# Kernel optimization log

Measured on AMD Instinct MI355X. Metric: run time of the kernel, lower is better.

Reference implementation:

```python
import jax, jax.numpy as jnp
import numpy as np

S, B, E, H = 2048, 2, 1024, 16
D = E // H  # head_dim = 64


def setup_inputs() -> dict:
    key = jax.random.key(0)
    ks = jax.random.split(key, 5)
    sp = (2.0 / (E + E)) ** 0.5  # xavier-ish scale
    return {
        "x": jax.random.normal(ks[0], (S, B, E), dtype=jnp.float32),
        "wq": jax.random.normal(ks[1], (E, E), dtype=jnp.float32) * sp,
        "bq": jnp.zeros((E,), jnp.float32),
        "wk": jax.random.normal(ks[2], (E, E), dtype=jnp.float32) * sp,
        "bk": jnp.zeros((E,), jnp.float32),
        "wv": jax.random.normal(ks[3], (E, E), dtype=jnp.float32) * sp,
        "bv": jnp.zeros((E,), jnp.float32),
        "wo": jax.random.normal(ks[4], (E, E), dtype=jnp.float32) * sp,
        "bo": jnp.zeros((E,), jnp.float32),
    }


def reference(x, wq, bq, wk, bk, wv, bv, wo, bo):
    # x: (S, B, E), weights in torch Linear convention (out, in)
    scaling = jnp.float32(D ** -0.5)
    q = (jnp.einsum('ibe,fe->ibf', x, wq) + bq) * scaling
    k = jnp.einsum('ibe,fe->ibf', x, wk) + bk
    v = jnp.einsum('ibe,fe->ibf', x, wv) + bv
    q = q.reshape(S, B, H, D)
    k = k.reshape(S, B, H, D)
    v = v.reshape(S, B, H, D)
    # energy: (B, H, S_q, S_k)
    energy = jnp.einsum('ibnf,jbnf->bnij', q, k)
    causal = jnp.triu(jnp.ones((S, S), dtype=bool), k=1)  # True above diagonal
    energy = jnp.where(causal[None, None], -jnp.inf, energy)
    weights = jax.nn.softmax(energy, axis=-1)
    head_ctx = jnp.einsum('bnij,jbnf->ibnf', weights, v)
    context = head_ctx.reshape(S, B, E)
    out = jnp.einsum('ibe,fe->ibf', context, wo) + bo
    return out
```

## Files before the change

kernel.cpp:

```cpp
#include <hip/hip_runtime.h>
#include <hip/hip_bf16.h>
#include <stdint.h>

#define S_LEN 2048
#define BATCH 2
#define EMB   1024
#define NH    16
#define HD    64
#define LOG2E 1.4426950408889634f

typedef __bf16 bf16x8 __attribute__((ext_vector_type(8)));
typedef float  f32x4  __attribute__((ext_vector_type(4)));
typedef unsigned short ushort8 __attribute__((ext_vector_type(8)));

__device__ __forceinline__ unsigned short f2bf(float f) {
  __bf16 h = (__bf16)f;
  return __builtin_bit_cast(unsigned short, h);
}

__device__ __forceinline__ ushort8 cvt8(const float4 a, const float4 b) {
  ushort8 o;
  o[0]=f2bf(a.x); o[1]=f2bf(a.y); o[2]=f2bf(a.z); o[3]=f2bf(a.w);
  o[4]=f2bf(b.x); o[5]=f2bf(b.y); o[6]=f2bf(b.z); o[7]=f2bf(b.w);
  return o;
}

__device__ __forceinline__ unsigned long long pack4(const f32x4 v) {
  return  (unsigned long long)f2bf(v[0])
       | ((unsigned long long)f2bf(v[1]) << 16)
       | ((unsigned long long)f2bf(v[2]) << 32)
       | ((unsigned long long)f2bf(v[3]) << 48);
}

#define GLOAD16(g, l) __builtin_amdgcn_global_load_lds( \
    (const __attribute__((address_space(1))) void*)(g),  \
    (__attribute__((address_space(3))) void*)(l), 16, 0, 0)

__global__ __launch_bounds__(256) void k_cvt(const float* __restrict__ src,
                                             unsigned short* __restrict__ dst,
                                             int n) {
  int i = (blockIdx.x*256 + threadIdx.x)*8;
  if (i >= n) return;
  const float4* s4 = (const float4*)(src + i);
  *(ushort8*)(dst + i) = cvt8(s4[0], s4[1]);
}

__global__ __launch_bounds__(256) void k_qkv_bb(
    const unsigned short* __restrict__ xb,
    const unsigned short* __restrict__ wb,
    const float* __restrict__ bq, const float* __restrict__ bk,
    const float* __restrict__ bv,
    unsigned short* __restrict__ Qb, unsigned short* __restrict__ Kb,
    unsigned short* __restrict__ Vtb)
{
  __shared__ unsigned short Al[128*32];
  __shared__ unsigned short Bl[128*32];
  const int tid = threadIdx.x;
  const int lin  = blockIdx.x;
  const int wgid = (lin & 7)*96 + (lin >> 3);
  const int mb   = wgid / 24;
  const int t    = wgid % 24;
  const int z    = t >> 3;
  const int nb   = t & 7;
  const int m0 = mb * 128;
  const int n0 = nb * 128;
  const int w = tid >> 6, lane = tid & 63;
  const int wr = w >> 1, wc = w & 1;
  const int lr = lane & 15, lhi = lane >> 4;
  const unsigned short* wz = wb + (size_t)z * (EMB*EMB);

  f32x4 acc[4][4];
#pragma unroll
  for (int m=0;m<4;++m)
#pragma unroll
    for (int n=0;n<4;++n) acc[m][n] = (f32x4){0.f,0.f,0.f,0.f};

  for (int k0 = 0; k0 < EMB; k0 += 32) {
    __syncthreads();
#pragma unroll
    for (int j = 0; j < 2; ++j) {
      const int c   = j*256 + tid;
      const int row = c >> 2;
      const int col = (c & 3) << 3;
      const int ub  = (j*256 + (tid & 192)) * 16;
      GLOAD16(xb + (size_t)(m0+row)*EMB + k0 + col, (char*)Al + ub);
      GLOAD16(wz + (size_t)(n0+row)*EMB + k0 + col, (char*)Bl + ub);
    }
    __syncthreads();
    bf16x8 af[4], bfr[4];
#pragma unroll
    for (int m=0;m<4;++m) af[m]  = *(const bf16x8*)&Al[(wr*64 + m*16 + lr)*32 + lhi*8];
#pragma unroll
    for (int n=0;n<4;++n) bfr[n] = *(const bf16x8*)&Bl[(wc*64 + n*16 + lr)*32 + lhi*8];
#pragma unroll
    for (int m=0;m<4;++m)
#pragma unroll
      for (int n=0;n<4;++n)
        acc[m][n] = __builtin_amdgcn_mfma_f32_16x16x32_bf16(af[m], bfr[n], acc[m][n], 0,0,0);
  }

  const float scale = (z==0) ? 0.125f*LOG2E : 1.0f;
  const float* bias = (z==0) ? bq : ((z==1) ? bk : bv);
#pragma unroll
  for (int m=0;m<4;++m)
#pragma unroll
    for (int n=0;n<4;++n)
#pragma unroll
      for (int r=0;r<4;++r) {
        const int rr   = m0 + wr*64 + m*16 + lhi*4 + r;
        const int fcol = n0 + wc*64 + n*16 + lr;
        const float v = (acc[m][n][r] + bias[fcol]) * scale;
        const unsigned short ov = f2bf(v);
        const int i = rr >> 1, bsel = rr & 1;
        const int h = fcol >> 6, d = fcol & 63;
        const int hh = bsel*NH + h;
        if (z == 0)      Qb [((size_t)hh*S_LEN + i)*HD + d] = ov;
        else if (z == 1) Kb [((size_t)hh*S_LEN + i)*HD + d] = ov;
        else             Vtb[((size_t)hh*HD + d)*S_LEN + i] = ov;
      }
}

__global__ __launch_bounds__(256) void k_qkv_bf(
    const unsigned short* __restrict__ xb,
    const float* __restrict__ wq, const float* __restrict__ wk,
    const float* __restrict__ wv,
    const float* __restrict__ bq, const float* __restrict__ bk,
    const float* __restrict__ bv,
    unsigned short* __restrict__ Qb, unsigned short* __restrict__ Kb,
    unsigned short* __restrict__ Vtb)
{
  __shared__ unsigned short Al[128*32];
  __shared__ unsigned short Bl[128*32];
  const int tid = threadIdx.x;
  const int lin  = blockIdx.x;
  const int wgid = (lin & 7)*96 + (lin >> 3);
  const int mb   = wgid / 24;
  const int t    = wgid % 24;
  const int z    = t >> 3;
  const int nb   = t & 7;
  const int m0 = mb * 128;
  const int n0 = nb * 128;
  const int w = tid >> 6, lane = tid & 63;
  const int wr = w >> 1, wc = w & 1;
  const int lr = lane & 15, lhi = lane >> 4;
  const float* wz = (z==0) ? wq : ((z==1) ? wk : wv);

  f32x4 acc[4][4];
#pragma unroll
  for (int m=0;m<4;++m)
#pragma unroll
    for (int n=0;n<4;++n) acc[m][n] = (f32x4){0.f,0.f,0.f,0.f};

  for (int k0 = 0; k0 < EMB; k0 += 32) {
    float4 b0[2], b1[2];
#pragma unroll
    for (int j = 0; j < 2; ++j) {
      const int c   = j*256 + tid;
      const int row = c >> 2;
      const int col = (c & 3) << 3;
      const float* bp = wz + (size_t)(n0+row)*EMB + k0 + col;
      b0[j] = *(const float4*)bp;  b1[j] = *(const float4*)(bp+4);
    }
    __syncthreads();
#pragma unroll
    for (int j = 0; j < 2; ++j) {
      const int c   = j*256 + tid;
      const int row = c >> 2;
      const int col = (c & 3) << 3;
      const int ub  = (j*256 + (tid & 192)) * 16;
      GLOAD16(xb + (size_t)(m0+row)*EMB + k0 + col, (char*)Al + ub);
      *(ushort8*)&Bl[row*32 + col] = cvt8(b0[j], b1[j]);
    }
    __syncthreads();
    bf16x8 af[4], bfr[4];
#pragma unroll
    for (int m=0;m<4;++m) af[m]  = *(const bf16x8*)&Al[(wr*64 + m*16 + lr)*32 + lhi*8];
#pragma unroll
    for (int n=0;n<4;++n) bfr[n] = *(const bf16x8*)&Bl[(wc*64 + n*16 + lr)*32 + lhi*8];
#pragma unroll
    for (int m=0;m<4;++m)
#pragma unroll
      for (int n=0;n<4;++n)
        acc[m][n] = __builtin_amdgcn_mfma_f32_16x16x32_bf16(af[m], bfr[n], acc[m][n], 0,0,0);
  }

  const float scale = (z==0) ? 0.125f*LOG2E : 1.0f;
  const float* bias = (z==0) ? bq : ((z==1) ? bk : bv);
#pragma unroll
  for (int m=0;m<4;++m)
#pragma unroll
    for (int n=0;n<4;++n)
#pragma unroll
      for (int r=0;r<4;++r) {
        const int rr   = m0 + wr*64 + m*16 + lhi*4 + r;
        const int fcol = n0 + wc*64 + n*16 + lr;
        const float v = (acc[m][n][r] + bias[fcol]) * scale;
        const unsigned short ov = f2bf(v);
        const int i = rr >> 1, bsel = rr & 1;
        const int h = fcol >> 6, d = fcol & 63;
        const int hh = bsel*NH + h;
        if (z == 0)      Qb [((size_t)hh*S_LEN + i)*HD + d] = ov;
        else if (z == 1) Kb [((size_t)hh*S_LEN + i)*HD + d] = ov;
        else             Vtb[((size_t)hh*HD + d)*S_LEN + i] = ov;
      }
}

__global__ __launch_bounds__(256) void k_qkv(
    const float* __restrict__ xA, int a_rs, int ishift,
    const float* __restrict__ wq, const float* __restrict__ wk,
    const float* __restrict__ wv,
    const float* __restrict__ bq, const float* __restrict__ bk,
    const float* __restrict__ bv,
    unsigned short* __restrict__ Qb, unsigned short* __restrict__ Kb,
    unsigned short* __restrict__ Vtb)
{
  __shared__ unsigned short Al[128*32];
  __shared__ unsigned short Bl[128*32];
  const int tid = threadIdx.x;
  const int z  = blockIdx.z;
  const int m0 = blockIdx.x * 128;
  const int n0 = blockIdx.y * 128;
  const int w = tid >> 6, lane = tid & 63;
  const int wr = w >> 1, wc = w & 1;
  const int lr = lane & 15, lhi = lane >> 4;
  const float* wz = (z==0) ? wq : ((z==1) ? wk : wv);

  f32x4 acc[4][4];
#pragma unroll
  for (int m=0;m<4;++m)
#pragma unroll
    for (int n=0;n<4;++n) acc[m][n] = (f32x4){0.f,0.f,0.f,0.f};

  for (int k0 = 0; k0 < EMB; k0 += 32) {
    float4 a0[2], a1[2], b0[2], b1[2];
#pragma unroll
    for (int j = 0; j < 2; ++j) {
      const int c   = j*256 + tid;
      const int row = c >> 2;
      const int col = (c & 3) << 3;
      const float* ap = xA + (size_t)(m0+row)*a_rs + k0 + col;
      const float* bp = wz + (size_t)(n0+row)*EMB + k0 + col;
      a0[j] = *(const float4*)ap;  a1[j] = *(const float4*)(ap+4);
      b0[j] = *(const float4*)bp;  b1[j] = *(const float4*)(bp+4);
    }
    __syncthreads();
#pragma unroll
    for (int j = 0; j < 2; ++j) {
      const int c   = j*256 + tid;
      const int row = c >> 2;
      const int col = (c & 3) << 3;
      *(ushort8*)&Al[row*32 + col] = cvt8(a0[j], a1[j]);
      *(ushort8*)&Bl[row*32 + col] = cvt8(b0[j], b1[j]);
    }
    __syncthreads();
    bf16x8 af[4], bfr[4];
#pragma unroll
    for (int m=0;m<4;++m) af[m]  = *(const bf16x8*)&Al[(wr*64 + m*16 + lr)*32 + lhi*8];
#pragma unroll
    for (int n=0;n<4;++n) bfr[n] = *(const bf16x8*)&Bl[(wc*64 + n*16 + lr)*32 + lhi*8];
#pragma unroll
    for (int m=0;m<4;++m)
#pragma unroll
      for (int n=0;n<4;++n)
        acc[m][n] = __builtin_amdgcn_mfma_f32_16x16x32_bf16(af[m], bfr[n], acc[m][n], 0,0,0);
  }

  const float scale = (z==0) ? 0.125f*LOG2E : 1.0f;
  const float* bias = (z==0) ? bq : ((z==1) ? bk : bv);
  const int bmask = (1 << ishift) - 1;
#pragma unroll
  for (int m=0;m<4;++m)
#pragma unroll
    for (int n=0;n<4;++n)
#pragma unroll
      for (int r=0;r<4;++r) {
        const int rr   = m0 + wr*64 + m*16 + lhi*4 + r;
        const int fcol = n0 + wc*64 + n*16 + lr;
        const float v = (acc[m][n][r] + bias[fcol]) * scale;
        const unsigned short ov = f2bf(v);
        const int i = rr >> ishift, bsel = rr & bmask;
        const int h = fcol >> 6, d = fcol & 63;
        const int hh = bsel*NH + h;
        if (z == 0)      Qb [((size_t)hh*S_LEN + i)*HD + d] = ov;
        else if (z == 1) Kb [((size_t)hh*S_LEN + i)*HD + d] = ov;
        else             Vtb[((size_t)hh*HD + d)*S_LEN + i] = ov;
      }
}

__global__ __launch_bounds__(256,4) void k_attn(
    const unsigned short* __restrict__ Q,
    const unsigned short* __restrict__ K,
    const unsigned short* __restrict__ Vt,
    unsigned short* __restrict__ ctx, int bshift, int hsh)
{
  __shared__ unsigned short KL[2][64*64];
  __shared__ unsigned short VL[2][64*64];
  __shared__ unsigned short Pl[4][16*64];

  const int tid = threadIdx.x;
  const int w = tid >> 6, lane = tid & 63;
  const int lr = lane & 15, lhi = lane >> 4;

  const int lin = blockIdx.x;
  const int cc  = lin >> hsh;
  const int chunk = (cc < 16) ? cc : (47 - cc);
  const int hh  = lin & ((1 << hsh) - 1);
  const int q0  = chunk*64 + w*16;

  const unsigned short* Qh = Q  + (size_t)hh*S_LEN*HD;
  const unsigned short* Kh = K  + (size_t)hh*S_LEN*HD;
  const unsigned short* Vh = Vt + (size_t)hh*HD*S_LEN;
  char* Pw = (char*)Pl[w];

  const int xm = (lr & 7) << 4;
  int kvb[2];
#pragma unroll
  for (int kf=0;kf<2;++kf) kvb[kf] = lr*128 + ((kf*64 + lhi*16) ^ xm);
  int pwb[4];
#pragma unroll
  for (int kn=0;kn<4;++kn)
    pwb[kn] = lr*128 + ((kn*32 + lhi*8) ^ xm);

  const unsigned short* kga[2];
  const unsigned short* vga[2];
#pragma unroll
  for (int j=0;j<2;++j) {
    const int c   = j*256 + tid;
    const int row = c >> 3;
    const int sb  = (c*16) ^ ((row & 7) << 4);
    const int el  = (sb & 127) >> 1;
    kga[j] = Kh + (size_t)row*HD + el;
    vga[j] = Vh + (size_t)row*S_LEN + el;
  }
  const int ub0 = (tid & 192) * 16;

  bf16x8 qf[2];
#pragma unroll
  for (int kf=0;kf<2;++kf)
    qf[kf] = *(const bf16x8*)&Qh[(size_t)(q0 + lr)*HD + kf*32 + lhi*8];

  f32x4 o[4];
  float rm = -3.0e38f, rl = 0.f;
#pragma unroll
  for (int dn=0;dn<4;++dn) o[dn] = (f32x4){0.f,0.f,0.f,0.f};

  const int tmax = chunk + 1;

  auto STAGE = [&](int tt, int bb2) {
#pragma unroll
    for (int j=0;j<2;++j) {
      GLOAD16(kga[j] + (size_t)tt*4096, (char*)KL[bb2] + ub0 + j*4096);
      GLOAD16(vga[j] + (size_t)tt*64,   (char*)VL[bb2] + ub0 + j*4096);
    }
  };

  STAGE(0, 0);
  int bb = 0;
  for (int t = 0; t < tmax; ++t) {
    if (t + 1 < tmax) {
      STAGE(t+1, bb^1);
      asm volatile("s_waitcnt vmcnt(4)" ::: "memory");
    } else {
      asm volatile("s_waitcnt vmcnt(0)" ::: "memory");
    }
    __builtin_amdgcn_s_barrier();

    const int kv0 = t*64;
    const char* KB = (const char*)KL[bb];
    const char* VB = (const char*)VL[bb];

    f32x4 st[4];
#pragma unroll
    for (int kn=0;kn<4;++kn) st[kn] = (f32x4){0.f,0.f,0.f,0.f};

    __builtin_amdgcn_s_setprio(1);
#pragma unroll
    for (int kn=0;kn<4;++kn)
#pragma unroll
      for (int kf=0;kf<2;++kf) {
        const bf16x8 kfr = *(const bf16x8*)(KB + kvb[kf] + kn*2048);
        st[kn] = __builtin_amdgcn_mfma_f32_16x16x32_bf16(kfr, qf[kf], st[kn], 0,0,0);
      }
    __builtin_amdgcn_s_setprio(0);

    if (t == tmax-1) {
      const int q = q0 + lr;
#pragma unroll
      for (int kn=0;kn<4;++kn)
#pragma unroll
        for (int r=0;r<4;++r) {
          const int k = kv0 + kn*16 + lhi*4 + r;
          if (k > q) st[kn][r] = -1.0e30f;
        }
    }

    float mx = fmaxf(fmaxf(st[0][0], st[0][1]), fmaxf(st[0][2], st[0][3]));
#pragma unroll
    for (int kn=1;kn<4;++kn)
      mx = fmaxf(mx, fmaxf(fmaxf(st[kn][0], st[kn][1]),
                           fmaxf(st[kn][2], st[kn][3])));
    mx = fmaxf(mx, __shfl_xor(mx, 16));
    mx = fmaxf(mx, __shfl_xor(mx, 32));
    if (!__all(mx - rm <= 8.0f)) {
      const float newm  = fmaxf(rm, mx);
      const float alpha = exp2f(rm - newm);
      rl *= alpha;
#pragma unroll
      for (int dn=0;dn<4;++dn)
#pragma unroll
        for (int r=0;r<4;++r) o[dn][r] *= alpha;
      rm = newm;
    }
    float sum = 0.f;
#pragma unroll
    for (int kn=0;kn<4;++kn)
#pragma unroll
      for (int r=0;r<4;++r) {
        const float p = exp2f(st[kn][r] - rm);
        st[kn][r] = p;
        sum += p;
      }
    sum += __shfl_xor(sum, 16);
    sum += __shfl_xor(sum, 32);
    rl += sum;

#pragma unroll
    for (int kn=0;kn<4;++kn)
      *(unsigned long long*)(Pw + pwb[kn]) = pack4(st[kn]);

#pragma unroll
    for (int ks=0;ks<2;++ks) {
      const bf16x8 pfr = *(const bf16x8*)(Pw + kvb[ks]);
      __builtin_amdgcn_s_setprio(1);
#pragma unroll
      for (int dn=0;dn<4;++dn) {
        const bf16x8 vf = *(const bf16x8*)(VB + kvb[ks] + dn*2048);
        o[dn] = __builtin_amdgcn_mfma_f32_16x16x32_bf16(vf, pfr, o[dn], 0,0,0);
      }
      __builtin_amdgcn_s_setprio(0);
    }

    __builtin_amdgcn_s_barrier();
    bb ^= 1;
  }

  const int h = hh & (NH-1);
  const int badd = hh >> 4;
  const float inv = 1.0f / rl;
  const int q = q0 + lr;
  const size_t trow = ((size_t)q << bshift) + badd;
#pragma unroll
  for (int dn=0;dn<4;++dn) {
    f32x4 ov;
#pragma unroll
    for (int r=0;r<4;++r) ov[r] = o[dn][r]*inv;
    *(unsigned long long*)&ctx[trow*EMB + h*HD + dn*16 + lhi*4] = pack4(ov);
  }
}

__global__ __launch_bounds__(256) void k_oproj_bf(
    const unsigned short* __restrict__ ctxA,
    const unsigned short* __restrict__ wob,
    const float* __restrict__ bo,
    float* __restrict__ out)
{
  __shared__ unsigned short Al[128*32];
  __shared__ unsigned short Bl[128*32];
  const int tid = threadIdx.x;
  const int m0 = blockIdx.x * 128;
  const int n0 = blockIdx.y * 128;
  const int w = tid >> 6, lane = tid & 63;
  const int wr = w >> 1, wc = w & 1;
  const int lr = lane & 15, lhi = lane >> 4;

  f32x4 acc[4][4];
#pragma unroll
  for (int m=0;m<4;++m)
#pragma unroll
    for (int n=0;n<4;++n) acc[m][n] = (f32x4){0.f,0.f,0.f,0.f};

  for (int k0 = 0; k0 < EMB; k0 += 32) {
    __syncthreads();
#pragma unroll
    for (int j = 0; j < 2; ++j) {
      const int c   = j*256 + tid;
      const int row = c >> 2;
      const int col = (c & 3) << 3;
      const int ub  = (j*256 + (tid & 192)) * 16;
      GLOAD16(ctxA + (size_t)(m0+row)*EMB + k0 + col, (char*)Al + ub);
      GLOAD16(wob  + (size_t)(n0+row)*EMB + k0 + col, (char*)Bl + ub);
    }
    __syncthreads();
    bf16x8 af[4], bfr[4];
#pragma unroll
    for (int m=0;m<4;++m) af[m]  = *(const bf16x8*)&Al[(wr*64 + m*16 + lr)*32 + lhi*8];
#pragma unroll
    for (int n=0;n<4;++n) bfr[n] = *(const bf16x8*)&Bl[(wc*64 + n*16 + lr)*32 + lhi*8];
#pragma unroll
    for (int m=0;m<4;++m)
#pragma unroll
      for (int n=0;n<4;++n)
        acc[m][n] = __builtin_amdgcn_mfma_f32_16x16x32_bf16(af[m], bfr[n], acc[m][n], 0,0,0);
  }

#pragma unroll
  for (int m=0;m<4;++m)
#pragma unroll
    for (int n=0;n<4;++n)
#pragma unroll
      for (int r=0;r<4;++r) {
        const int rr   = m0 + wr*64 + m*16 + lhi*4 + r;
        const int fcol = n0 + wc*64 + n*16 + lr;
        out[(size_t)rr*EMB + fcol] = acc[m][n][r] + bo[fcol];
      }
}

__global__ __launch_bounds__(256) void k_oproj(
    const unsigned short* __restrict__ ctxA,
    const float* __restrict__ wo,
    const float* __restrict__ bo,
    float* __restrict__ outb, int orm)
{
  __shared__ unsigned short Al[128*32];
  __shared__ unsigned short Bl[128*32];
  const int tid = threadIdx.x;
  const int m0 = blockIdx.x * 128;
  const int n0 = blockIdx.y * 128;
  const int w = tid >> 6, lane = tid & 63;
  const int wr = w >> 1, wc = w & 1;
  const int lr = lane & 15, lhi = lane >> 4;

  f32x4 acc[4][4];
#pragma unroll
  for (int m=0;m<4;++m)
#pragma unroll
    for (int n=0;n<4;++n) acc[m][n] = (f32x4){0.f,0.f,0.f,0.f};

  for (int k0 = 0; k0 < EMB; k0 += 32) {
    float4 b0[2], b1[2];
#pragma unroll
    for (int j = 0; j < 2; ++j) {
      const int c   = j*256 + tid;
      const int row = c >> 2;
      const int col = (c & 3) << 3;
      const float* bp = wo + (size_t)(n0+row)*EMB + k0 + col;
      b0[j] = *(const float4*)bp;  b1[j] = *(const float4*)(bp+4);
    }
    __syncthreads();
#pragma unroll
    for (int j = 0; j < 2; ++j) {
      const int c   = j*256 + tid;
      const int row = c >> 2;
      const int col = (c & 3) << 3;
      const int ub  = (j*256 + (tid & 192)) * 16;
      GLOAD16(ctxA + (size_t)(m0+row)*EMB + k0 + col, (char*)Al + ub);
      *(ushort8*)&Bl[row*32 + col] = cvt8(b0[j], b1[j]);
    }
    __syncthreads();
    bf16x8 af[4], bfr[4];
#pragma unroll
    for (int m=0;m<4;++m) af[m]  = *(const bf16x8*)&Al[(wr*64 + m*16 + lr)*32 + lhi*8];
#pragma unroll
    for (int n=0;n<4;++n) bfr[n] = *(const bf16x8*)&Bl[(wc*64 + n*16 + lr)*32 + lhi*8];
#pragma unroll
    for (int m=0;m<4;++m)
#pragma unroll
      for (int n=0;n<4;++n)
        acc[m][n] = __builtin_amdgcn_mfma_f32_16x16x32_bf16(af[m], bfr[n], acc[m][n], 0,0,0);
  }

#pragma unroll
  for (int m=0;m<4;++m)
#pragma unroll
    for (int n=0;n<4;++n)
#pragma unroll
      for (int r=0;r<4;++r) {
        const int rr   = m0 + wr*64 + m*16 + lhi*4 + r;
        const int fcol = n0 + wc*64 + n*16 + lr;
        outb[(size_t)rr*orm*EMB + fcol] = acc[m][n][r] + bo[fcol];
      }
}

extern "C" void kernel_launch(void* const* d_in, const int* in_sizes, int n_in,
                              void* d_out, int out_size, void* d_ws, size_t ws_size,
                              hipStream_t stream) {
  const float* x  = (const float*)d_in[0];
  const float* wq = (const float*)d_in[1];
  const float* bq = (const float*)d_in[2];
  const float* wk = (const float*)d_in[3];
  const float* bk = (const float*)d_in[4];
  const float* wv = (const float*)d_in[5];
  const float* bv = (const float*)d_in[6];
  const float* wo = (const float*)d_in[7];
  const float* bo = (const float*)d_in[8];
  float* out = (float*)d_out;

  char* ws = (char*)d_ws;
  const size_t MB = (size_t)1 << 20;

  if (ws_size >= 38*MB) {
    unsigned short* Q   = (unsigned short*)(ws + 0*MB);
    unsigned short* K   = (unsigned short*)(ws + 8*MB);
    unsigned short* Vt  = (unsigned short*)(ws + 16*MB);
    unsigned short* wb  = (unsigned short*)(ws + 24*MB);
    unsigned short* xb  = (unsigned short*)(ws + 30*MB);
    unsigned short* cx  = (unsigned short*)(ws + 24*MB);
    unsigned short* wob = Vt;

    k_cvt<<<2048, 256, 0, stream>>>(x,  xb, (S_LEN*BATCH)*EMB);
    k_cvt<<<512,  256, 0, stream>>>(wq, wb + (size_t)0*EMB*EMB, EMB*EMB);
    k_cvt<<<512,  256, 0, stream>>>(wk, wb + (size_t)1*EMB*EMB, EMB*EMB);
    k_cvt<<<512,  256, 0, stream>>>(wv, wb + (size_t)2*EMB*EMB, EMB*EMB);
    k_qkv_bb<<<768, 256, 0, stream>>>(xb, wb, bq,bk,bv, Q, K, Vt);
    k_attn<<<1024, 256, 0, stream>>>(Q, K, Vt, cx, 1, 5);
    k_cvt<<<512, 256, 0, stream>>>(wo, wob, EMB*EMB);
    k_oproj_bf<<<dim3(32,8), 256, 0, stream>>>(cx, wob, bo, out);
  } else if (ws_size >= 32*MB) {
    unsigned short* Q   = (unsigned short*)(ws + 0*MB);
    unsigned short* K   = (unsigned short*)(ws + 8*MB);
    unsigned short* Vt  = (unsigned short*)(ws + 16*MB);
    unsigned short* cx  = (unsigned short*)(ws + 24*MB);
    unsigned short* xb  = cx;
    unsigned short* wob = Vt;

    k_cvt<<<2048, 256, 0, stream>>>(x, xb, (S_LEN*BATCH)*EMB);
    k_qkv_bf<<<768, 256, 0, stream>>>(xb, wq,wk,wv, bq,bk,bv, Q, K, Vt);
    k_attn<<<1024, 256, 0, stream>>>(Q, K, Vt, cx, 1, 5);
    k_cvt<<<512, 256, 0, stream>>>(wo, wob, EMB*EMB);
    k_oproj_bf<<<dim3(32,8), 256, 0, stream>>>(cx, wob, bo, out);
  } else {
    unsigned short* Q  = (unsigned short*)(ws + 0*MB);
    unsigned short* K  = (unsigned short*)(ws + 4*MB);
    unsigned short* Vt = (unsigned short*)(ws + 8*MB);
    unsigned short* cx = (unsigned short*)(ws + 12*MB);
    for (int b = 0; b < 2; ++b) {
      k_qkv<<<dim3(16,8,3), 256, 0, stream>>>(x + b*EMB, 2*EMB, 0,
                                              wq,wk,wv, bq,bk,bv, Q,K,Vt);
      k_attn<<<512, 256, 0, stream>>>(Q, K, Vt, cx, 0, 4);
      k_oproj<<<dim3(16,8), 256, 0, stream>>>(cx, wo, bo, out + b*EMB, 2);
    }
  }
}
```

Baseline: 131.7 us.

## Double-buffer LDS in projection GEMMs and merge fp32-to-bf16 conversion launches

The QKV and output projection GEMMs now use two LDS buffers, prefetching the next K-tile with global_load_lds while computing on the current one. Explicit vmcnt waits and raw barriers replace the two __syncthreads per iteration, and MFMA sections are raised in priority with s_setprio. Separately, the four conversion kernels for x, wq, wk and wv are merged into a single launch to cut launch overhead. LDS use per block doubles, which may reduce occupancy, and correctness now depends on the hand-counted vmcnt value.

```diff
diff --git a/kernel.cpp b/kernel.cpp
--- a/kernel.cpp
+++ b/kernel.cpp
@@ -41,6 +41,28 @@
                                              int n) {
   int i = (blockIdx.x*256 + threadIdx.x)*8;
   if (i >= n) return;
+  const float4* s4 = (const float4*)(src + i);
+  *(ushort8*)(dst + i) = cvt8(s4[0], s4[1]);
+}
+
+__global__ __launch_bounds__(256) void k_cvt_all(
+    const float* __restrict__ x,
+    const float* __restrict__ wq, const float* __restrict__ wk,
+    const float* __restrict__ wv,
+    unsigned short* __restrict__ xb, unsigned short* __restrict__ wb) {
+  const int b = blockIdx.x;
+  const float* src;
+  unsigned short* dst;
+  int off;
+  if (b < 2048) { src = x; dst = xb; off = b; }
+  else {
+    const int t = b - 2048;
+    const int z = t >> 9;
+    src = (z==0) ? wq : ((z==1) ? wk : wv);
+    dst = wb + (size_t)z*EMB*EMB;
+    off = t & 511;
+  }
+  const int i = (off*256 + threadIdx.x)*8;
   const float4* s4 = (const float4*)(src + i);
   *(ushort8*)(dst + i) = cvt8(s4[0], s4[1]);
 }
@@ -53,8 +75,8 @@
     unsigned short* __restrict__ Qb, unsigned short* __restrict__ Kb,
     unsigned short* __restrict__ Vtb)
 {
-  __shared__ unsigned short Al[128*32];
-  __shared__ unsigned short Bl[128*32];
+  __shared__ unsigned short Al[2][128*32];
+  __shared__ unsigned short Bl[2][128*32];
   const int tid = threadIdx.x;
   const int lin  = blockIdx.x;
   const int wgid = (lin & 7)*96 + (lin >> 3);
@@ -69,34 +91,59 @@
   const int lr = lane & 15, lhi = lane >> 4;
   const unsigned short* wz = wb + (size_t)z * (EMB*EMB);
 
+  const unsigned short* ag[2];
+  const unsigned short* bg[2];
+  int ub[2];
+#pragma unroll
+  for (int j=0;j<2;++j) {
+    const int c   = j*256 + tid;
+    const int row = c >> 2;
+    const int col = (c & 3) << 3;
+    ag[j] = xb + (size_t)(m0+row)*EMB + col;
+    bg[j] = wz + (size_t)(n0+row)*EMB + col;
+    ub[j] = (j*256 + (tid & 192)) * 16;
+  }
+
+  auto STAGE = [&](int k0, int b2) {
+#pragma unroll
+    for (int j=0;j<2;++j) {
+      GLOAD16(ag[j] + k0, (char*)Al[b2] + ub[j]);
+      GLOAD16(bg[j] + k0, (char*)Bl[b2] + ub[j]);
+    }
+  };
+
   f32x4 acc[4][4];
 #pragma unroll
   for (int m=0;m<4;++m)
 #pragma unroll
     for (int n=0;n<4;++n) acc[m][n] = (f32x4){0.f,0.f,0.f,0.f};
 
+  STAGE(0, 0);
+  int bbuf = 0;
   for (int k0 = 0; k0 < EMB; k0 += 32) {
-    __syncthreads();
-#pragma unroll
-    for (int j = 0; j < 2; ++j) {
-      const int c   = j*256 + tid;
-      const int row = c >> 2;
-      const int col = (c & 3) << 3;
-      const int ub  = (j*256 + (tid & 192)) * 16;
-      GLOAD16(xb + (size_t)(m0+row)*EMB + k0 + col, (char*)Al + ub);
-      GLOAD16(wz + (size_t)(n0+row)*EMB + k0 + col, (char*)Bl + ub);
-    }
-    __syncthreads();
+    if (k0 + 32 < EMB) {
+      STAGE(k0 + 32, bbuf^1);
+      asm volatile("s_waitcnt vmcnt(4)" ::: "memory");
+    } else {
+      asm volatile("s_waitcnt vmcnt(0)" ::: "memory");
+    }
+    __builtin_amdgcn_s_barrier();
+
     bf16x8 af[4], bfr[4];
 #pragma unroll
-    for (int m=0;m<4;++m) af[m]  = *(const bf16x8*)&Al[(wr*64 + m*16 + lr)*32 + lhi*8];
-#pragma unroll
-    for (int n=0;n<4;++n) bfr[n] = *(const bf16x8*)&Bl[(wc*64 + n*16 + lr)*32 + lhi*8];
+    for (int m=0;m<4;++m) af[m]  = *(const bf16x8*)&Al[bbuf][(wr*64 + m*16 + lr)*32 + lhi*8];
+#pragma unroll
+    for (int n=0;n<4;++n) bfr[n] = *(const bf16x8*)&Bl[bbuf][(wc*64 + n*16 + lr)*32 + lhi*8];
+    __builtin_amdgcn_s_setprio(1);
 #pragma unroll
     for (int m=0;m<4;++m)
 #pragma unroll
       for (int n=0;n<4;++n)
         acc[m][n] = __builtin_amdgcn_mfma_f32_16x16x32_bf16(af[m], bfr[n], acc[m][n], 0,0,0);
+    __builtin_amdgcn_s_setprio(0);
+
+    __builtin_amdgcn_s_barrier();
+    bbuf ^= 1;
   }
 
   const float scale = (z==0) ? 0.125f*LOG2E : 1.0f;
@@ -464,8 +511,8 @@
     const float* __restrict__ bo,
     float* __restrict__ out)
 {
-  __shared__ unsigned short Al[128*32];
-  __shared__ unsigned short Bl[128*32];
+  __shared__ unsigned short Al[2][128*32];
+  __shared__ unsigned short Bl[2][128*32];
   const int tid = threadIdx.x;
   const int m0 = blockIdx.x * 128;
   const int n0 = blockIdx.y * 128;
@@ -473,34 +520,59 @@
   const int wr = w >> 1, wc = w & 1;
   const int lr = lane & 15, lhi = lane >> 4;
 
+  const unsigned short* ag[2];
+  const unsigned short* bg[2];
+  int ub[2];
+#pragma unroll
+  for (int j=0;j<2;++j) {
+    const int c   = j*256 + tid;
+    const int row = c >> 2;
+    const int col = (c & 3) << 3;
+    ag[j] = ctxA + (size_t)(m0+row)*EMB + col;
+    bg[j] = wob  + (size_t)(n0+row)*EMB + col;
+    ub[j] = (j*256 + (tid & 192)) * 16;
+  }
+
+  auto STAGE = [&](int k0, int b2) {
+#pragma unroll
+    for (int j=0;j<2;++j) {
+      GLOAD16(ag[j] + k0, (char*)Al[b2] + ub[j]);
+      GLOAD16(bg[j] + k0, (char*)Bl[b2] + ub[j]);
+    }
+  };
+
   f32x4 acc[4][4];
 #pragma unroll
   for (int m=0;m<4;++m)
 #pragma unroll
     for (int n=0;n<4;++n) acc[m][n] = (f32x4){0.f,0.f,0.f,0.f};
 
+  STAGE(0, 0);
+  int bbuf = 0;
   for (int k0 = 0; k0 < EMB; k0 += 32) {
-    __syncthreads();
-#pragma unroll
-    for (int j = 0; j < 2; ++j) {
-      const int c   = j*256 + tid;
-      const int row = c >> 2;
-      const int col = (c & 3) << 3;
-      const int ub  = (j*256 + (tid & 192)) * 16;
-      GLOAD16(ctxA + (size_t)(m0+row)*EMB + k0 + col, (char*)Al + ub);
-      GLOAD16(wob  + (size_t)(n0+row)*EMB + k0 + col, (char*)Bl + ub);
-    }
-    __syncthreads();
+    if (k0 + 32 < EMB) {
+      STAGE(k0 + 32, bbuf^1);
+      asm volatile("s_waitcnt vmcnt(4)" ::: "memory");
+    } else {
+      asm volatile("s_waitcnt vmcnt(0)" ::: "memory");
+    }
+    __builtin_amdgcn_s_barrier();
+
     bf16x8 af[4], bfr[4];
 #pragma unroll
-    for (int m=0;m<4;++m) af[m]  = *(const bf16x8*)&Al[(wr*64 + m*16 + lr)*32 + lhi*8];
-#pragma unroll
-    for (int n=0;n<4;++n) bfr[n] = *(const bf16x8*)&Bl[(wc*64 + n*16 + lr)*32 + lhi*8];
+    for (int m=0;m<4;++m) af[m]  = *(const bf16x8*)&Al[bbuf][(wr*64 + m*16 + lr)*32 + lhi*8];
+#pragma unroll
+    for (int n=0;n<4;++n) bfr[n] = *(const bf16x8*)&Bl[bbuf][(wc*64 + n*16 + lr)*32 + lhi*8];
+    __builtin_amdgcn_s_setprio(1);
 #pragma unroll
     for (int m=0;m<4;++m)
 #pragma unroll
       for (int n=0;n<4;++n)
         acc[m][n] = __builtin_amdgcn_mfma_f32_16x16x32_bf16(af[m], bfr[n], acc[m][n], 0,0,0);
+    __builtin_amdgcn_s_setprio(0);
+
+    __builtin_amdgcn_s_barrier();
+    bbuf ^= 1;
   }
 
 #pragma unroll
@@ -607,10 +679,7 @@
     unsigned short* cx  = (unsigned short*)(ws + 24*MB);
     unsigned short* wob = Vt;
 
-    k_cvt<<<2048, 256, 0, stream>>>(x,  xb, (S_LEN*BATCH)*EMB);
-    k_cvt<<<512,  256, 0, stream>>>(wq, wb + (size_t)0*EMB*EMB, EMB*EMB);
-    k_cvt<<<512,  256, 0, stream>>>(wk, wb + (size_t)1*EMB*EMB, EMB*EMB);
-    k_cvt<<<512,  256, 0, stream>>>(wv, wb + (size_t)2*EMB*EMB, EMB*EMB);
+    k_cvt_all<<<3584, 256, 0, stream>>>(x, wq, wk, wv, xb, wb);
     k_qkv_bb<<<768, 256, 0, stream>>>(xb, wb, bq,bk,bv, Q, K, Vt);
     k_attn<<<1024, 256, 0, stream>>>(Q, K, Vt, cx, 1, 5);
     k_cvt<<<512, 256, 0, stream>>>(wo, wob, EMB*EMB);
```

After: 126.4 us. 4.0% less time.
